# Performance work log

Hardware: AMD Instinct MI355X
Metric: run time of the kernel (lower is better)

Reference implementation:

```python
import jax, jax.numpy as jnp
import numpy as np

N, E = 50000, 800000
IN_CH, HID, OUT = 128, 64, 64
H1, H2 = 4, 1
NEG_SLOPE = 0.2  # PyG GATConv default


def _glorot(key, shape):
    fan_in, fan_out = shape[0], shape[-1]
    lim = (6.0 / (fan_in + fan_out)) ** 0.5
    return jax.random.uniform(key, shape, jnp.float32, -lim, lim)


def setup_inputs() -> dict:
    key = jax.random.key(0)
    ks = jax.random.split(key, 12)
    x = jax.random.normal(ks[0], (N, IN_CH), jnp.float32)
    edge_index = jax.random.randint(ks[1], (2, E), 0, N, jnp.int64)
    # layer 1: in_ch -> hid, 4 heads, concat
    W1 = _glorot(ks[2], (IN_CH, H1 * HID))
    a_src1 = _glorot(ks[3], (H1, HID))
    a_dst1 = _glorot(ks[4], (H1, HID))
    b1 = jnp.zeros((H1 * HID,), jnp.float32)
    # layer 2: hid*4 -> out, 1 head, mean (concat=False)
    W2 = _glorot(ks[5], (H1 * HID, H2 * OUT))
    a_src2 = _glorot(ks[6], (H2, OUT))
    a_dst2 = _glorot(ks[7], (H2, OUT))
    b2 = jnp.zeros((OUT,), jnp.float32)
    return {"x": x, "edge_index": edge_index, "W1": W1, "a_src1": a_src1,
            "a_dst1": a_dst1, "b1": b1, "W2": W2, "a_src2": a_src2,
            "a_dst2": a_dst2, "b2": b2}


def gat_layer(x, src, dst, W, a_src, a_dst, b, concat):
    n = x.shape[0]
    Hh, Fh = a_src.shape
    h = (x @ W).reshape(n, Hh, Fh)                      # [N,H,F]
    al_src = jnp.sum(h * a_src[None], axis=-1)          # [N,H]
    al_dst = jnp.sum(h * a_dst[None], axis=-1)          # [N,H]
    logits = jax.nn.leaky_relu(al_src[src] + al_dst[dst], NEG_SLOPE)  # [E,H]
    # numerically stable segment softmax over destination nodes
    mx = jax.ops.segment_max(logits, dst, num_segments=n)
    mx = jnp.where(jnp.isfinite(mx), mx, 0.0)
    e = jnp.exp(logits - mx[dst])                       # [E,H]
    denom = jax.ops.segment_sum(e, dst, num_segments=n)  # [N,H]
    alpha = e / jnp.maximum(denom[dst], 1e-16)          # [E,H]
    msg = h[src] * alpha[:, :, None]                    # [E,H,F]
    out = jax.ops.segment_sum(msg, dst, num_segments=n)  # [N,H,F]
    out = out.reshape(n, Hh * Fh) if concat else out.mean(axis=1)
    return out + b


def reference(x, edge_index, W1, a_src1, a_dst1, b1, W2, a_src2, a_dst2, b2):
    n = x.shape[0]
    # PyG GATConv adds self-loops by default
    loops = jnp.arange(n, dtype=edge_index.dtype)
    src = jnp.concatenate([edge_index[0], loops])
    dst = jnp.concatenate([edge_index[1], loops])
    h = gat_layer(x, src, dst, W1, a_src1, a_dst1, b1, concat=True)
    h = jax.nn.elu(h)
    # dropout is identity in eval mode
    out = gat_layer(h, src, dst, W2, a_src2, a_dst2, b2, concat=False)
    return out
```

## Files before the change

kernel.cpp:

```cpp
#include <hip/hip_runtime.h>
#include <math.h>

#define NEG_SLOPE 0.2f
#define SLOTS 128

typedef unsigned short ushort_t;
typedef _Float16 f16x8 __attribute__((ext_vector_type(8)));
typedef _Float16 h2v  __attribute__((ext_vector_type(2)));
typedef float f32x4v __attribute__((ext_vector_type(4)));

__device__ __forceinline__ float leaky(float x) { return x > 0.f ? x : NEG_SLOPE * x; }

__device__ __forceinline__ ushort_t f2h(float f) {
    union { _Float16 h; ushort_t u; } v; v.h = (_Float16)f; return v.u;
}
__device__ __forceinline__ float h2f(ushort_t u) {
    union { ushort_t u; _Float16 h; } v; v.u = u; return (float)v.h;
}
__device__ __forceinline__ unsigned packh(float a, float b) {
    union { h2v h; unsigned u; } c; c.h[0] = (_Float16)a; c.h[1] = (_Float16)b; return c.u;
}

__global__ __launch_bounds__(256) void k_prep1(const int* __restrict__ ei, int E, int EB4,
                                               int* __restrict__ cnt, ushort_t* __restrict__ csr,
                                               const float* __restrict__ W1, const float* __restrict__ W2,
                                               const float* __restrict__ as1, const float* __restrict__ ad1,
                                               const float* __restrict__ as2, const float* __restrict__ ad2,
                                               ushort_t* __restrict__ W1t, ushort_t* __restrict__ W2t,
                                               float* __restrict__ va1s, float* __restrict__ va1d,
                                               float* __restrict__ va2s, float* __restrict__ va2d, int N) {
    int b = blockIdx.x;
    int t = threadIdx.x;
    if (b < EB4) {
        int i = (b * 256 + t) * 4;
        if (i + 3 < E) {
            int4 s4 = *(const int4*)(ei + i);
            int4 d4 = *(const int4*)(ei + E + i);
            int p;
            p = atomicAdd(&cnt[d4.x], 1); if (p < SLOTS - 1) csr[d4.x * SLOTS + 1 + p] = (ushort_t)s4.x;
            p = atomicAdd(&cnt[d4.y], 1); if (p < SLOTS - 1) csr[d4.y * SLOTS + 1 + p] = (ushort_t)s4.y;
            p = atomicAdd(&cnt[d4.z], 1); if (p < SLOTS - 1) csr[d4.z * SLOTS + 1 + p] = (ushort_t)s4.z;
            p = atomicAdd(&cnt[d4.w], 1); if (p < SLOTS - 1) csr[d4.w * SLOTS + 1 + p] = (ushort_t)s4.w;
        } else {
            for (int k = i; k < E; ++k) {
                int d = ei[E + k];
                int p = atomicAdd(&cnt[d], 1);
                if (p < SLOTS - 1) csr[d * SLOTS + 1 + p] = (ushort_t)ei[k];
            }
        }
        return;
    }
    b -= EB4;
    if (b < 256) {
        if (t < 128) W1t[b * 128 + t] = f2h(W1[t * 256 + b]);
        return;
    } else if (b < 320) {
        int n = b - 256;
        W2t[n * 256 + t] = f2h(W2[t * 64 + n]);
        return;
    } else if (b == 320) {
        for (int idx = t; idx < 1024; idx += 256) {
            int k = idx >> 3, h = (idx >> 1) & 3, sd = idx & 1;
            const float* a = sd ? ad1 : as1;
            float acc = 0.f;
            for (int f = 0; f < 64; ++f) acc += W1[k * 256 + h * 64 + f] * a[h * 64 + f];
            (sd ? va1d : va1s)[k * 4 + h] = acc;
        }
        return;
    } else if (b == 321) {
        for (int idx = t; idx < 512; idx += 256) {
            int k = idx >> 1, sd = idx & 1;
            const float* a = sd ? ad2 : as2;
            float acc = 0.f;
            for (int f = 0; f < 64; ++f) acc += W2[k * 64 + f] * a[f];
            (sd ? va2d : va2s)[k] = acc;
        }
        return;
    }
    b -= 322;
    int n = b * 256 + t;
    if (n < N) csr[n * SLOTS] = (ushort_t)n;
}

__global__ __launch_bounds__(256) void k_gemm1(const float* __restrict__ x, const ushort_t* __restrict__ W1t,
                                               const float* __restrict__ va1s, const float* __restrict__ va1d,
                                               ushort_t* __restrict__ h1h,
                                               float4* __restrict__ alS, float4* __restrict__ alD, int N) {
    __shared__ ushort_t As[64 * 136];
    __shared__ ushort_t Bs[128 * 136];
    int t = threadIdx.x;
    int r0 = blockIdx.x * 64;
    int c0 = blockIdx.y * 128;
    #pragma unroll
    for (int q = 0; q < 4; ++q) {
        int idx = t + q * 256;
        int row = idx >> 4, off = idx & 15;
        int gr = r0 + row;
        uint4 pv = make_uint4(0, 0, 0, 0);
        if (gr < N) {
            const float* xp = x + (size_t)gr * 128 + off * 8;
            float4 f0 = *(const float4*)xp;
            float4 f1 = *(const float4*)(xp + 4);
            pv.x = packh(f0.x, f0.y); pv.y = packh(f0.z, f0.w);
            pv.z = packh(f1.x, f1.y); pv.w = packh(f1.z, f1.w);
        }
        *(uint4*)&As[row * 136 + off * 8] = pv;
    }
    #pragma unroll
    for (int q = 0; q < 8; ++q) {
        int idx = t + q * 256;
        int row = idx >> 4, off = idx & 15;
        uint4 v = *(const uint4*)(W1t + (size_t)(c0 + row) * 128 + off * 8);
        *(uint4*)&Bs[row * 136 + off * 8] = v;
    }
    __syncthreads();
    int w = t >> 6, lane = t & 63;
    int m = lane & 15, quad = lane >> 4;
    f32x4v acc[4][2];
    #pragma unroll
    for (int r = 0; r < 4; ++r)
        #pragma unroll
        for (int c = 0; c < 2; ++c)
            acc[r][c] = (f32x4v){0.f, 0.f, 0.f, 0.f};
    #pragma unroll
    for (int ks = 0; ks < 4; ++ks) {
        int k0 = ks * 32 + quad * 8;
        f16x8 af[4], bfr[2];
        #pragma unroll
        for (int r = 0; r < 4; ++r) af[r] = *(f16x8*)&As[(r * 16 + m) * 136 + k0];
        #pragma unroll
        for (int c = 0; c < 2; ++c) bfr[c] = *(f16x8*)&Bs[(w * 32 + c * 16 + m) * 136 + k0];
        #pragma unroll
        for (int r = 0; r < 4; ++r)
            #pragma unroll
            for (int c = 0; c < 2; ++c)
                acc[r][c] = __builtin_amdgcn_mfma_f32_16x16x32_f16(af[r], bfr[c], acc[r][c], 0, 0, 0);
    }
    #pragma unroll
    for (int r = 0; r < 4; ++r) {
        int gr0 = r0 + r * 16 + quad * 4;
        #pragma unroll
        for (int c = 0; c < 2; ++c) {
            int col = c0 + w * 32 + c * 16 + m;
            #pragma unroll
            for (int reg = 0; reg < 4; ++reg) {
                int gr = gr0 + reg;
                if (gr < N) h1h[(size_t)gr * 256 + col] = f2h(acc[r][c][reg]);
            }
        }
    }
    if (c0 == 0) {
        int r = t >> 2, kq = (t & 3) * 32;
        int gr = r0 + r;
        float s0 = 0, s1 = 0, s2 = 0, s3 = 0, d0 = 0, d1 = 0, d2 = 0, d3 = 0;
        for (int k = kq; k < kq + 32; ++k) {
            float xv = h2f(As[r * 136 + k]);
            float4 vs = *(const float4*)&va1s[k * 4];
            float4 vd = *(const float4*)&va1d[k * 4];
            s0 += xv * vs.x; s1 += xv * vs.y; s2 += xv * vs.z; s3 += xv * vs.w;
            d0 += xv * vd.x; d1 += xv * vd.y; d2 += xv * vd.z; d3 += xv * vd.w;
        }
        #pragma unroll
        for (int off = 1; off <= 2; off <<= 1) {
            s0 += __shfl_xor(s0, off, 64); s1 += __shfl_xor(s1, off, 64);
            s2 += __shfl_xor(s2, off, 64); s3 += __shfl_xor(s3, off, 64);
            d0 += __shfl_xor(d0, off, 64); d1 += __shfl_xor(d1, off, 64);
            d2 += __shfl_xor(d2, off, 64); d3 += __shfl_xor(d3, off, 64);
        }
        if ((t & 3) == 0 && gr < N) {
            alS[gr] = make_float4(s0, s1, s2, s3);
            alD[gr] = make_float4(d0, d1, d2, d3);
        }
    }
}

__global__ __launch_bounds__(256) void k_gemm2(const ushort_t* __restrict__ in, const ushort_t* __restrict__ W2t,
                                               ushort_t* __restrict__ h2h, int N) {
    __shared__ ushort_t As[64 * 136];
    __shared__ ushort_t Bs[64 * 136];
    int t = threadIdx.x;
    int r0 = blockIdx.x * 64;
    int w = t >> 6, lane = t & 63;
    int m = lane & 15, quad = lane >> 4;
    f32x4v acc[4];
    #pragma unroll
    for (int r = 0; r < 4; ++r) acc[r] = (f32x4v){0.f, 0.f, 0.f, 0.f};
    for (int kb = 0; kb < 2; ++kb) {
        #pragma unroll
        for (int q = 0; q < 4; ++q) {
            int idx = t + q * 256;
            int row = idx >> 4, off = idx & 15;
            int gr = r0 + row;
            uint4 v = (gr < N) ? *(const uint4*)(in + (size_t)gr * 256 + kb * 128 + off * 8)
                               : make_uint4(0, 0, 0, 0);
            *(uint4*)&As[row * 136 + off * 8] = v;
        }
        #pragma unroll
        for (int q = 0; q < 4; ++q) {
            int idx = t + q * 256;
            int row = idx >> 4, off = idx & 15;
            uint4 v = *(const uint4*)(W2t + (size_t)row * 256 + kb * 128 + off * 8);
            *(uint4*)&Bs[row * 136 + off * 8] = v;
        }
        __syncthreads();
        #pragma unroll
        for (int ks = 0; ks < 4; ++ks) {
            int k0 = ks * 32 + quad * 8;
            f16x8 af[4], bfr;
            #pragma unroll
            for (int r = 0; r < 4; ++r) af[r] = *(f16x8*)&As[(r * 16 + m) * 136 + k0];
            bfr = *(f16x8*)&Bs[(w * 16 + m) * 136 + k0];
            #pragma unroll
            for (int r = 0; r < 4; ++r)
                acc[r] = __builtin_amdgcn_mfma_f32_16x16x32_f16(af[r], bfr, acc[r], 0, 0, 0);
        }
        __syncthreads();
    }
    int col = w * 16 + m;
    #pragma unroll
    for (int r = 0; r < 4; ++r) {
        int gr0 = r0 + r * 16 + quad * 4;
        #pragma unroll
        for (int reg = 0; reg < 4; ++reg) {
            int gr = gr0 + reg;
            if (gr < N) h2h[(size_t)gr * 64 + col] = f2h(acc[r][reg]);
        }
    }
}

__global__ __launch_bounds__(256) void k_agg1(const int* __restrict__ cnt, const ushort_t* __restrict__ csr,
                                              const float4* __restrict__ alS4, const float4* __restrict__ alD4,
                                              const ushort_t* __restrict__ h1h, const float* __restrict__ b1,
                                              const float* __restrict__ va2s, const float* __restrict__ va2d,
                                              ushort_t* __restrict__ out1h,
                                              float* __restrict__ al2S, float* __restrict__ al2D, int N) {
    __shared__ float s_alpha[4][SLOTS + 1][4];
    __shared__ int   s_off[4][SLOTS + 1];
    int w = threadIdx.x >> 6, lane = threadIdx.x & 63;
    int n = blockIdx.x * 4 + w;
    if (n >= N) return;
    int stored = cnt[n]; if (stored > SLOTS - 1) stored = SLOTS - 1;
    int deg = stored + 1;
    const ushort_t* crow = csr + (size_t)n * SLOTS;
    float4 ald = alD4[n];

    float d0 = 0.f, d1 = 0.f, d2 = 0.f, d3 = 0.f;
    for (int j = lane; j < deg; j += 64) {
        int s = crow[j];
        float4 as = alS4[s];
        float e0 = __expf(leaky(as.x + ald.x));
        float e1 = __expf(leaky(as.y + ald.y));
        float e2 = __expf(leaky(as.z + ald.z));
        float e3 = __expf(leaky(as.w + ald.w));
        s_off[w][j] = s << 9;
        *(float4*)&s_alpha[w][j][0] = make_float4(e0, e1, e2, e3);
        d0 += e0; d1 += e1; d2 += e2; d3 += e3;
    }
    if (lane == 0) {
        s_off[w][deg] = 0;
        *(float4*)&s_alpha[w][deg][0] = make_float4(0.f, 0.f, 0.f, 0.f);
    }
    #pragma unroll
    for (int off = 32; off >= 1; off >>= 1) {
        d0 += __shfl_xor(d0, off, 64);
        d1 += __shfl_xor(d1, off, 64);
        d2 += __shfl_xor(d2, off, 64);
        d3 += __shfl_xor(d3, off, 64);
    }
    int half = lane >> 5, lid = lane & 31;
    int head = lid >> 3;
    float denh = head == 0 ? d0 : head == 1 ? d1 : head == 2 ? d2 : d3;
    float invh = 1.f / fmaxf(denh, 1e-16f);

    const char* hbase = (const char*)h1h;
    int choff = lid * 16;
    float facc[8] = {0.f, 0.f, 0.f, 0.f, 0.f, 0.f, 0.f, 0.f};
    for (int j0 = 0; j0 < deg; j0 += 8) {
        h2v ha0 = (h2v)0, ha1 = (h2v)0, ha2 = (h2v)0, ha3 = (h2v)0;
        int jmax = (j0 + 8 < deg) ? j0 + 8 : deg;
        for (int j = j0; j < jmax; j += 2) {
            int jj = j + half;
            float a = s_alpha[w][jj][head];
            int o = s_off[w][jj];
            union { uint4 u; h2v h[4]; } c;
            c.u = *(const uint4*)(hbase + o + choff);
            _Float16 ah = (_Float16)a;
            h2v a2 = {ah, ah};
            ha0 += c.h[0] * a2;
            ha1 += c.h[1] * a2;
            ha2 += c.h[2] * a2;
            ha3 += c.h[3] * a2;
        }
        facc[0] += (float)ha0[0]; facc[1] += (float)ha0[1];
        facc[2] += (float)ha1[0]; facc[3] += (float)ha1[1];
        facc[4] += (float)ha2[0]; facc[5] += (float)ha2[1];
        facc[6] += (float)ha3[0]; facc[7] += (float)ha3[1];
    }
    #pragma unroll
    for (int i = 0; i < 8; ++i) facc[i] += __shfl_xor(facc[i], 32, 64);

    int c8 = lid * 8;
    float4 bv0 = *(const float4*)&b1[c8];
    float4 bv1 = *(const float4*)&b1[c8 + 4];
    float v[8];
    v[0] = facc[0] * invh + bv0.x; v[1] = facc[1] * invh + bv0.y;
    v[2] = facc[2] * invh + bv0.z; v[3] = facc[3] * invh + bv0.w;
    v[4] = facc[4] * invh + bv1.x; v[5] = facc[5] * invh + bv1.y;
    v[6] = facc[6] * invh + bv1.z; v[7] = facc[7] * invh + bv1.w;
    #pragma unroll
    for (int i = 0; i < 8; ++i) v[i] = v[i] > 0.f ? v[i] : (__expf(v[i]) - 1.f);
    float4 vs0 = *(const float4*)&va2s[c8], vs1 = *(const float4*)&va2s[c8 + 4];
    float4 vd0 = *(const float4*)&va2d[c8], vd1 = *(const float4*)&va2d[c8 + 4];
    float ps = v[0]*vs0.x + v[1]*vs0.y + v[2]*vs0.z + v[3]*vs0.w
             + v[4]*vs1.x + v[5]*vs1.y + v[6]*vs1.z + v[7]*vs1.w;
    float pd = v[0]*vd0.x + v[1]*vd0.y + v[2]*vd0.z + v[3]*vd0.w
             + v[4]*vd1.x + v[5]*vd1.y + v[6]*vd1.z + v[7]*vd1.w;
    #pragma unroll
    for (int off = 16; off >= 1; off >>= 1) {
        ps += __shfl_xor(ps, off, 64);
        pd += __shfl_xor(pd, off, 64);
    }
    if (lane == 0) { al2S[n] = ps; al2D[n] = pd; }
    if (half == 0) {
        uint4 u;
        u.x = packh(v[0], v[1]); u.y = packh(v[2], v[3]);
        u.z = packh(v[4], v[5]); u.w = packh(v[6], v[7]);
        *(uint4*)(out1h + (size_t)n * 256 + c8) = u;
    }
}

__global__ __launch_bounds__(256) void k_agg2(const int* __restrict__ cnt, const ushort_t* __restrict__ csr,
                                              const float* __restrict__ alS, const float* __restrict__ alD,
                                              const ushort_t* __restrict__ h2h, const float* __restrict__ b2,
                                              float* __restrict__ out, int N) {
    int lane = threadIdx.x & 63;
    int n = blockIdx.x * 4 + (threadIdx.x >> 6);
    if (n >= N) return;
    int stored = cnt[n]; if (stored > SLOTS - 1) stored = SLOTS - 1;
    int deg = stored + 1;
    const ushort_t* crow = csr + (size_t)n * SLOTS;
    float ald = alD[n];

    int s0 = 0; float e0 = 0.f;
    int s1 = 0; float e1 = 0.f;
    float den = 0.f;
    for (int j = lane; j < deg; j += 64) {
        int s = crow[j];
        float e = __expf(leaky(alS[s] + ald));
        if (j < 64) { s0 = s; e0 = e; } else { s1 = s; e1 = e; }
        den += e;
    }
    #pragma unroll
    for (int off = 32; off >= 1; off >>= 1) den += __shfl_xor(den, off, 64);
    float inv = 1.f / fmaxf(den, 1e-16f);

    int grp = lane >> 3, cid = lane & 7;
    int choff = cid * 16;
    const char* hbase = (const char*)h2h;
    h2v ha0 = (h2v)0, ha1 = (h2v)0, ha2 = (h2v)0, ha3 = (h2v)0;
    int lim = deg < 64 ? deg : 64;
    for (int j = 0; j < lim; j += 8) {
        int jj = j + grp;
        float a = __shfl(e0, jj, 64);
        int s = __shfl(s0, jj, 64);
        if (jj > 63) a = 0.f;
        union { uint4 u; h2v h[4]; } c;
        c.u = *(const uint4*)(hbase + (s << 7) + choff);
        _Float16 ah = (_Float16)a;
        h2v a2 = {ah, ah};
        ha0 += c.h[0] * a2; ha1 += c.h[1] * a2;
        ha2 += c.h[2] * a2; ha3 += c.h[3] * a2;
    }
    for (int j = 64; j < deg; j += 8) {
        int rel = j - 64 + grp;
        float a = __shfl(e1, rel, 64);
        int s = __shfl(s1, rel, 64);
        if (rel > 63) a = 0.f;
        union { uint4 u; h2v h[4]; } c;
        c.u = *(const uint4*)(hbase + (s << 7) + choff);
        _Float16 ah = (_Float16)a;
        h2v a2 = {ah, ah};
        ha0 += c.h[0] * a2; ha1 += c.h[1] * a2;
        ha2 += c.h[2] * a2; ha3 += c.h[3] * a2;
    }
    float acc[8];
    acc[0] = (float)ha0[0]; acc[1] = (float)ha0[1];
    acc[2] = (float)ha1[0]; acc[3] = (float)ha1[1];
    acc[4] = (float)ha2[0]; acc[5] = (float)ha2[1];
    acc[6] = (float)ha3[0]; acc[7] = (float)ha3[1];
    #pragma unroll
    for (int off = 8; off <= 32; off <<= 1)
        #pragma unroll
        for (int i = 0; i < 8; ++i) acc[i] += __shfl_xor(acc[i], off, 64);

    if (grp == 0) {
        int c8 = cid * 8;
        float4 b0 = *(const float4*)&b2[c8];
        float4 b1v = *(const float4*)&b2[c8 + 4];
        float4 o0 = make_float4(acc[0]*inv + b0.x, acc[1]*inv + b0.y, acc[2]*inv + b0.z, acc[3]*inv + b0.w);
        float4 o1 = make_float4(acc[4]*inv + b1v.x, acc[5]*inv + b1v.y, acc[6]*inv + b1v.z, acc[7]*inv + b1v.w);
        *(float4*)(out + (size_t)n * 64 + c8) = o0;
        *(float4*)(out + (size_t)n * 64 + c8 + 4) = o1;
    }
}

extern "C" void kernel_launch(void* const* d_in, const int* in_sizes, int n_in,
                              void* d_out, int out_size, void* d_ws, size_t ws_size,
                              hipStream_t stream) {
    const float* x      = (const float*)d_in[0];
    const int*   ei     = (const int*)d_in[1];
    const float* W1     = (const float*)d_in[2];
    const float* a_src1 = (const float*)d_in[3];
    const float* a_dst1 = (const float*)d_in[4];
    const float* b1     = (const float*)d_in[5];
    const float* W2     = (const float*)d_in[6];
    const float* a_src2 = (const float*)d_in[7];
    const float* a_dst2 = (const float*)d_in[8];
    const float* b2     = (const float*)d_in[9];
    float* out = (float*)d_out;

    int N = in_sizes[0] / 128;
    int E = in_sizes[1] / 2;

    char* ws = (char*)d_ws;
    size_t off = 0;
    auto alloc = [&](size_t bytes) -> void* {
        void* p = ws + off;
        off = (off + bytes + 255) & ~(size_t)255;
        return p;
    };
    ushort_t* h1h   = (ushort_t*)alloc((size_t)N * 256 * 2);
    ushort_t* out1h = (ushort_t*)alloc((size_t)N * 256 * 2);
    ushort_t* h2h   = (ushort_t*)alloc((size_t)N * 64 * 2);
    ushort_t* W1t   = (ushort_t*)alloc(256 * 128 * 2);
    ushort_t* W2t   = (ushort_t*)alloc(64 * 256 * 2);
    float* va1s  = (float*)alloc(128 * 4 * 4);
    float* va1d  = (float*)alloc(128 * 4 * 4);
    float* va2s  = (float*)alloc(256 * 4);
    float* va2d  = (float*)alloc(256 * 4);
    float* alS1  = (float*)alloc((size_t)N * 4 * 4);
    float* alD1  = (float*)alloc((size_t)N * 4 * 4);
    float* alS2  = (float*)alloc((size_t)N * 4);
    float* alD2  = (float*)alloc((size_t)N * 4);
    int*   cnt   = (int*)alloc((size_t)N * 4);
    ushort_t* csr = (ushort_t*)alloc((size_t)N * SLOTS * 2);
    (void)ws_size; (void)n_in; (void)out_size;

    int EB4 = (E / 4 + 255) / 256;
    int NB  = (N + 255) / 256;
    int GB1 = (N + 63) / 64;

    hipMemsetAsync(cnt, 0, (size_t)N * 4, stream);

    k_prep1<<<EB4 + 322 + NB, 256, 0, stream>>>(ei, E, EB4, cnt, csr,
                                                W1, W2, a_src1, a_dst1, a_src2, a_dst2,
                                                W1t, W2t, va1s, va1d, va2s, va2d, N);
    dim3 g1(GB1, 2);
    k_gemm1<<<g1, 256, 0, stream>>>(x, W1t, va1s, va1d, h1h,
                                    (float4*)alS1, (float4*)alD1, N);
    k_agg1<<<(N + 3) / 4, 256, 0, stream>>>(cnt, csr,
                                            (const float4*)alS1, (const float4*)alD1,
                                            h1h, b1, va2s, va2d, out1h, alS2, alD2, N);
    k_gemm2<<<GB1, 256, 0, stream>>>(out1h, W2t, h2h, N);
    k_agg2<<<(N + 3) / 4, 256, 0, stream>>>(cnt, csr, alS2, alD2, h2h, b2, out, N);
}
```

Before: 280.4 us.

## Fuse layer-2 projection GEMM into layer-1 aggregation kernel and batch gathers

Removes the separate MFMA GEMM2 kernel and the out1h intermediate. Each wavefront now writes its ELU'd 256-wide row to LDS and computes the 64 layer-2 outputs with scalar packed-half dot products against W2t, deriving the attention logits from those outputs. The neighbour gather loop is also restructured to issue four gathers before accumulating. This saves one launch and an N×256 fp16 round trip through global memory. In exchange, k_agg1 does 256×64 per-lane FMAs from global W2t without tensor cores, and the fp16 accumulation order changes.

```diff
diff --git a/kernel.cpp b/kernel.cpp
--- a/kernel.cpp
+++ b/kernel.cpp
@@ -25,10 +25,8 @@
                                                int* __restrict__ cnt, ushort_t* __restrict__ csr,
                                                const float* __restrict__ W1, const float* __restrict__ W2,
                                                const float* __restrict__ as1, const float* __restrict__ ad1,
-                                               const float* __restrict__ as2, const float* __restrict__ ad2,
                                                ushort_t* __restrict__ W1t, ushort_t* __restrict__ W2t,
-                                               float* __restrict__ va1s, float* __restrict__ va1d,
-                                               float* __restrict__ va2s, float* __restrict__ va2d, int N) {
+                                               float* __restrict__ va1s, float* __restrict__ va1d, int N) {
     int b = blockIdx.x;
     int t = threadIdx.x;
     if (b < EB4) {
@@ -67,17 +65,8 @@
             (sd ? va1d : va1s)[k * 4 + h] = acc;
         }
         return;
-    } else if (b == 321) {
-        for (int idx = t; idx < 512; idx += 256) {
-            int k = idx >> 1, sd = idx & 1;
-            const float* a = sd ? ad2 : as2;
-            float acc = 0.f;
-            for (int f = 0; f < 64; ++f) acc += W2[k * 64 + f] * a[f];
-            (sd ? va2d : va2s)[k] = acc;
-        }
-        return;
-    }
-    b -= 322;
+    }
+    b -= 321;
     int n = b * 256 + t;
     if (n < N) csr[n * SLOTS] = (ushort_t)n;
 }
@@ -174,68 +163,16 @@
     }
 }
 
-__global__ __launch_bounds__(256) void k_gemm2(const ushort_t* __restrict__ in, const ushort_t* __restrict__ W2t,
-                                               ushort_t* __restrict__ h2h, int N) {
-    __shared__ ushort_t As[64 * 136];
-    __shared__ ushort_t Bs[64 * 136];
-    int t = threadIdx.x;
-    int r0 = blockIdx.x * 64;
-    int w = t >> 6, lane = t & 63;
-    int m = lane & 15, quad = lane >> 4;
-    f32x4v acc[4];
-    #pragma unroll
-    for (int r = 0; r < 4; ++r) acc[r] = (f32x4v){0.f, 0.f, 0.f, 0.f};
-    for (int kb = 0; kb < 2; ++kb) {
-        #pragma unroll
-        for (int q = 0; q < 4; ++q) {
-            int idx = t + q * 256;
-            int row = idx >> 4, off = idx & 15;
-            int gr = r0 + row;
-            uint4 v = (gr < N) ? *(const uint4*)(in + (size_t)gr * 256 + kb * 128 + off * 8)
-                               : make_uint4(0, 0, 0, 0);
-            *(uint4*)&As[row * 136 + off * 8] = v;
-        }
-        #pragma unroll
-        for (int q = 0; q < 4; ++q) {
-            int idx = t + q * 256;
-            int row = idx >> 4, off = idx & 15;
-            uint4 v = *(const uint4*)(W2t + (size_t)row * 256 + kb * 128 + off * 8);
-            *(uint4*)&Bs[row * 136 + off * 8] = v;
-        }
-        __syncthreads();
-        #pragma unroll
-        for (int ks = 0; ks < 4; ++ks) {
-            int k0 = ks * 32 + quad * 8;
-            f16x8 af[4], bfr;
-            #pragma unroll
-            for (int r = 0; r < 4; ++r) af[r] = *(f16x8*)&As[(r * 16 + m) * 136 + k0];
-            bfr = *(f16x8*)&Bs[(w * 16 + m) * 136 + k0];
-            #pragma unroll
-            for (int r = 0; r < 4; ++r)
-                acc[r] = __builtin_amdgcn_mfma_f32_16x16x32_f16(af[r], bfr, acc[r], 0, 0, 0);
-        }
-        __syncthreads();
-    }
-    int col = w * 16 + m;
-    #pragma unroll
-    for (int r = 0; r < 4; ++r) {
-        int gr0 = r0 + r * 16 + quad * 4;
-        #pragma unroll
-        for (int reg = 0; reg < 4; ++reg) {
-            int gr = gr0 + reg;
-            if (gr < N) h2h[(size_t)gr * 64 + col] = f2h(acc[r][reg]);
-        }
-    }
-}
-
 __global__ __launch_bounds__(256) void k_agg1(const int* __restrict__ cnt, const ushort_t* __restrict__ csr,
                                               const float4* __restrict__ alS4, const float4* __restrict__ alD4,
                                               const ushort_t* __restrict__ h1h, const float* __restrict__ b1,
-                                              const float* __restrict__ va2s, const float* __restrict__ va2d,
-                                              ushort_t* __restrict__ out1h,
+                                              const ushort_t* __restrict__ W2t,
+                                              const float* __restrict__ as2, const float* __restrict__ ad2,
+                                              ushort_t* __restrict__ h2h,
                                               float* __restrict__ al2S, float* __restrict__ al2D, int N) {
     __shared__ float s_alpha[4][SLOTS + 1][4];
     __shared__ int   s_off[4][SLOTS + 1];
+    __shared__ unsigned s_row[4][128];
     int w = threadIdx.x >> 6, lane = threadIdx.x & 63;
     int n = blockIdx.x * 4 + w;
     if (n >= N) return;
@@ -275,21 +212,40 @@
     const char* hbase = (const char*)h1h;
     int choff = lid * 16;
     float facc[8] = {0.f, 0.f, 0.f, 0.f, 0.f, 0.f, 0.f, 0.f};
-    for (int j0 = 0; j0 < deg; j0 += 8) {
+    int j0 = 0;
+    for (; j0 + 8 <= deg; j0 += 8) {
+        uint4 pbuf[4]; float abuf[4];
+        #pragma unroll
+        for (int i = 0; i < 4; ++i) {
+            int jj = j0 + i * 2 + half;
+            abuf[i] = s_alpha[w][jj][head];
+            pbuf[i] = *(const uint4*)(hbase + s_off[w][jj] + choff);
+        }
         h2v ha0 = (h2v)0, ha1 = (h2v)0, ha2 = (h2v)0, ha3 = (h2v)0;
-        int jmax = (j0 + 8 < deg) ? j0 + 8 : deg;
-        for (int j = j0; j < jmax; j += 2) {
+        #pragma unroll
+        for (int i = 0; i < 4; ++i) {
+            union { uint4 u; h2v h[4]; } c; c.u = pbuf[i];
+            _Float16 ah = (_Float16)abuf[i];
+            h2v a2 = {ah, ah};
+            ha0 += c.h[0] * a2; ha1 += c.h[1] * a2;
+            ha2 += c.h[2] * a2; ha3 += c.h[3] * a2;
+        }
+        facc[0] += (float)ha0[0]; facc[1] += (float)ha0[1];
+        facc[2] += (float)ha1[0]; facc[3] += (float)ha1[1];
+        facc[4] += (float)ha2[0]; facc[5] += (float)ha2[1];
+        facc[6] += (float)ha3[0]; facc[7] += (float)ha3[1];
+    }
+    if (j0 < deg) {
+        h2v ha0 = (h2v)0, ha1 = (h2v)0, ha2 = (h2v)0, ha3 = (h2v)0;
+        for (int j = j0; j < deg; j += 2) {
             int jj = j + half;
             float a = s_alpha[w][jj][head];
-            int o = s_off[w][jj];
             union { uint4 u; h2v h[4]; } c;
-            c.u = *(const uint4*)(hbase + o + choff);
+            c.u = *(const uint4*)(hbase + s_off[w][jj] + choff);
             _Float16 ah = (_Float16)a;
             h2v a2 = {ah, ah};
-            ha0 += c.h[0] * a2;
-            ha1 += c.h[1] * a2;
-            ha2 += c.h[2] * a2;
-            ha3 += c.h[3] * a2;
+            ha0 += c.h[0] * a2; ha1 += c.h[1] * a2;
+            ha2 += c.h[2] * a2; ha3 += c.h[3] * a2;
         }
         facc[0] += (float)ha0[0]; facc[1] += (float)ha0[1];
         facc[2] += (float)ha1[0]; facc[3] += (float)ha1[1];
@@ -309,24 +265,36 @@
     v[6] = facc[6] * invh + bv1.z; v[7] = facc[7] * invh + bv1.w;
     #pragma unroll
     for (int i = 0; i < 8; ++i) v[i] = v[i] > 0.f ? v[i] : (__expf(v[i]) - 1.f);
-    float4 vs0 = *(const float4*)&va2s[c8], vs1 = *(const float4*)&va2s[c8 + 4];
-    float4 vd0 = *(const float4*)&va2d[c8], vd1 = *(const float4*)&va2d[c8 + 4];
-    float ps = v[0]*vs0.x + v[1]*vs0.y + v[2]*vs0.z + v[3]*vs0.w
-             + v[4]*vs1.x + v[5]*vs1.y + v[6]*vs1.z + v[7]*vs1.w;
-    float pd = v[0]*vd0.x + v[1]*vd0.y + v[2]*vd0.z + v[3]*vd0.w
-             + v[4]*vd1.x + v[5]*vd1.y + v[6]*vd1.z + v[7]*vd1.w;
-    #pragma unroll
-    for (int off = 16; off >= 1; off >>= 1) {
+
+    if (half == 0) {
+        s_row[w][lid * 4 + 0] = packh(v[0], v[1]);
+        s_row[w][lid * 4 + 1] = packh(v[2], v[3]);
+        s_row[w][lid * 4 + 2] = packh(v[4], v[5]);
+        s_row[w][lid * 4 + 3] = packh(v[6], v[7]);
+    }
+    const ushort_t* w2row = W2t + (size_t)lane * 256;
+    float hc = 0.f;
+    #pragma unroll
+    for (int cch = 0; cch < 16; ++cch) {
+        h2v hacc = (h2v)0;
+        #pragma unroll
+        for (int p = 0; p < 8; ++p) {
+            int pp = cch * 8 + p;
+            union { unsigned u; h2v h; } rp; rp.u = s_row[w][pp];
+            h2v wp = *(const h2v*)&w2row[pp * 2];
+            hacc += rp.h * wp;
+        }
+        hc += (float)hacc[0] + (float)hacc[1];
+    }
+    float ps = hc * as2[lane];
+    float pd = hc * ad2[lane];
+    #pragma unroll
+    for (int off = 32; off >= 1; off >>= 1) {
         ps += __shfl_xor(ps, off, 64);
         pd += __shfl_xor(pd, off, 64);
     }
     if (lane == 0) { al2S[n] = ps; al2D[n] = pd; }
-    if (half == 0) {
-        uint4 u;
-        u.x = packh(v[0], v[1]); u.y = packh(v[2], v[3]);
-        u.z = packh(v[4], v[5]); u.w = packh(v[6], v[7]);
-        *(uint4*)(out1h + (size_t)n * 256 + c8) = u;
-    }
+    h2h[(size_t)n * 64 + lane] = f2h(hc);
 }
 
 __global__ __launch_bounds__(256) void k_agg2(const int* __restrict__ cnt, const ushort_t* __restrict__ csr,
@@ -430,14 +398,11 @@
         return p;
     };
     ushort_t* h1h   = (ushort_t*)alloc((size_t)N * 256 * 2);
-    ushort_t* out1h = (ushort_t*)alloc((size_t)N * 256 * 2);
     ushort_t* h2h   = (ushort_t*)alloc((size_t)N * 64 * 2);
     ushort_t* W1t   = (ushort_t*)alloc(256 * 128 * 2);
     ushort_t* W2t   = (ushort_t*)alloc(64 * 256 * 2);
     float* va1s  = (float*)alloc(128 * 4 * 4);
     float* va1d  = (float*)alloc(128 * 4 * 4);
-    float* va2s  = (float*)alloc(256 * 4);
-    float* va2d  = (float*)alloc(256 * 4);
     float* alS1  = (float*)alloc((size_t)N * 4 * 4);
     float* alD1  = (float*)alloc((size_t)N * 4 * 4);
     float* alS2  = (float*)alloc((size_t)N * 4);
@@ -452,15 +417,15 @@
 
     hipMemsetAsync(cnt, 0, (size_t)N * 4, stream);
 
-    k_prep1<<<EB4 + 322 + NB, 256, 0, stream>>>(ei, E, EB4, cnt, csr,
-                                                W1, W2, a_src1, a_dst1, a_src2, a_dst2,
-                                                W1t, W2t, va1s, va1d, va2s, va2d, N);
+    k_prep1<<<EB4 + 321 + NB, 256, 0, stream>>>(ei, E, EB4, cnt, csr,
+                                                W1, W2, a_src1, a_dst1,
+                                                W1t, W2t, va1s, va1d, N);
     dim3 g1(GB1, 2);
     k_gemm1<<<g1, 256, 0, stream>>>(x, W1t, va1s, va1d, h1h,
                                     (float4*)alS1, (float4*)alD1, N);
     k_agg1<<<(N + 3) / 4, 256, 0, stream>>>(cnt, csr,
                                             (const float4*)alS1, (const float4*)alD1,
-                                            h1h, b1, va2s, va2d, out1h, alS2, alD2, N);
-    k_gemm2<<<GB1, 256, 0, stream>>>(out1h, W2t, h2h, N);
+                                            h1h, b1, W2t, a_src2, a_dst2,
+                                            h2h, alS2, alD2, N);
     k_agg2<<<(N + 3) / 4, 256, 0, stream>>>(cnt, csr, alS2, alD2, h2h, b2, out, N);
 }
```

Result: slower. 424.2 us (+51.3%).
